# Kernel tuning notes

Hardware: AMD Instinct MI355X
Metric: run time of the kernel (lower is better)

The kernel has to match this reference:

```python
import jax, jax.numpy as jnp
import numpy as np

N_HEADS, N_LEVELS, N_POINTS = 8, 4, 4


def _bilinear(im, grid, H, W):
    # im: [N, D, H*W] flattened level feature, grid: [N, Q, P, 2] in [-1, 1]
    # F.grid_sample bilinear, padding_mode='zeros', align_corners=False
    N, Q, P, _ = grid.shape
    D = im.shape[1]
    gx = ((grid[..., 0] + 1.0) * W - 1.0) * 0.5
    gy = ((grid[..., 1] + 1.0) * H - 1.0) * 0.5
    x0f = jnp.floor(gx)
    y0f = jnp.floor(gy)
    x0 = x0f.astype(jnp.int32)
    y0 = y0f.astype(jnp.int32)
    wx1 = gx - x0f
    wy1 = gy - y0f
    acc = jnp.zeros((N, D, Q * P), im.dtype)
    corners = ((0, 0, (1 - wx1) * (1 - wy1)), (1, 0, wx1 * (1 - wy1)),
               (0, 1, (1 - wx1) * wy1), (1, 1, wx1 * wy1))
    for dx, dy, wgt in corners:
        xi = x0 + dx
        yi = y0 + dy
        valid = (xi >= 0) & (xi < W) & (yi >= 0) & (yi < H)
        idx = jnp.clip(yi, 0, H - 1) * W + jnp.clip(xi, 0, W - 1)
        v = jnp.take_along_axis(im, idx.reshape(N, 1, Q * P), axis=2)  # [N,D,QP]
        acc = acc + v * jnp.where(valid, wgt, 0.0).reshape(N, 1, Q * P)
    return acc.reshape(N, D, Q, P)


def _forward(query, value, reference_points, shapes_np,
             w_off, b_off, w_attn, b_attn, w_val, b_val, w_out, b_out):
    B, Q, E = query.shape
    H_, L, P = N_HEADS, N_LEVELS, N_POINTS
    D = E // H_
    v = (value @ w_val + b_val).reshape(B, -1, H_, D)  # [B, Nv, H, D]
    off = (query @ w_off + b_off).reshape(B, Q, H_, L, P, 2)
    attn = (query @ w_attn + b_attn).reshape(B, Q, H_, L * P)
    attn = jax.nn.softmax(attn, axis=-1).reshape(B, Q, H_, L, P)
    # offset_scale = [W_l, H_l] per level
    scale = jnp.asarray(np.stack([shapes_np[:, 1], shapes_np[:, 0]], -1), jnp.float32)
    locs = reference_points[:, :, None, :, None, :] + off / scale[None, None, None, :, None, :]
    grid = 2.0 * locs - 1.0  # [B, Q, H, L, P, 2]
    starts = np.concatenate([[0], np.cumsum(shapes_np[:, 0] * shapes_np[:, 1])]).astype(int)
    out = jnp.zeros((B * H_, D, Q), query.dtype)
    for lvl in range(L):
        h, w = int(shapes_np[lvl, 0]), int(shapes_np[lvl, 1])
        feat = v[:, starts[lvl]:starts[lvl + 1]]                      # [B, h*w, H, D]
        feat = feat.transpose(0, 2, 3, 1).reshape(B * H_, D, h * w)   # [BH, D, hw]
        g = jnp.transpose(grid[:, :, :, lvl], (0, 2, 1, 3, 4)).reshape(B * H_, Q, P, 2)
        sampled = _bilinear(feat, g, h, w)                            # [BH, D, Q, P]
        wl = jnp.transpose(attn[:, :, :, lvl], (0, 2, 1, 3)).reshape(B * H_, 1, Q, P)
        out = out + (sampled * wl).sum(-1)                            # [BH, D, Q]
    out = out.reshape(B, H_ * D, Q).transpose(0, 2, 1)                # [B, Q, E]
    return out @ w_out + b_out


def setup_inputs() -> dict:
    key = jax.random.key(0)
    ks = jax.random.split(key, 12)
    B, Q, E = 2, 19947, 256
    L, H_, P = N_LEVELS, N_HEADS, N_POINTS
    shapes = jnp.array([[100, 150], [50, 75], [25, 38], [13, 19]], dtype=jnp.int64)
    s = 0.02
    return {
        'query': jax.random.normal(ks[0], (B, Q, E), jnp.float32),
        'value': jax.random.normal(ks[1], (B, Q, E), jnp.float32),
        'reference_points': jax.random.uniform(ks[2], (B, Q, L, 2), jnp.float32),
        'spatial_shapes': shapes,
        'w_off': jax.random.normal(ks[3], (E, H_ * L * P * 2), jnp.float32) * s,
        'b_off': jax.random.normal(ks[4], (H_ * L * P * 2,), jnp.float32) * s,
        'w_attn': jax.random.normal(ks[5], (E, H_ * L * P), jnp.float32) * s,
        'b_attn': jax.random.normal(ks[6], (H_ * L * P,), jnp.float32) * s,
        'w_val': jax.random.normal(ks[7], (E, E), jnp.float32) * s,
        'b_val': jax.random.normal(ks[8], (E,), jnp.float32) * s,
        'w_out': jax.random.normal(ks[9], (E, E), jnp.float32) * s,
        'b_out': jax.random.normal(ks[10], (E,), jnp.float32) * s,
    }


def reference(query, value, reference_points, spatial_shapes,
              w_off, b_off, w_attn, b_attn, w_val, b_val, w_out, b_out):
    shapes_np = np.asarray(spatial_shapes)
    return _forward(query, value, reference_points, shapes_np,
                    w_off, b_off, w_attn, b_attn, w_val, b_val, w_out, b_out)
```

## Files before the change

kernel.cpp:

```cpp
#include <hip/hip_runtime.h>
#include <math.h>

#define B_    2
#define Q_    19947
#define E_    256
#define H_    8
#define D_    32
#define L_    4
#define P_    4

typedef _Float16 f16_t;
typedef f16_t f16x8 __attribute__((ext_vector_type(8)));
typedef f16_t f16x4 __attribute__((ext_vector_type(4)));
typedef float f32x4 __attribute__((ext_vector_type(4)));

__global__ __launch_bounds__(256)
void transpose_all(const float* __restrict__ w_val, const float* __restrict__ w_off,
                   const float* __restrict__ w_attn, const float* __restrict__ w_out,
                   f16_t* __restrict__ WtV, f16_t* __restrict__ WtQ,
                   f16_t* __restrict__ WtO)
{
    const float* in; f16_t* out; int N;
    switch (blockIdx.z) {
        case 0:  in = w_val;  out = WtV;             N = 256; break;
        case 1:  in = w_off;  out = WtQ;             N = 256; break;
        case 2:  in = w_attn; out = WtQ + 256 * 256; N = 128; break;
        default: in = w_out;  out = WtO;             N = 256; break;
    }
    const int nt = blockIdx.x * 32;
    if (nt >= N) return;
    const int kt = blockIdx.y * 32;

    __shared__ float tile[32][33];
    const int x  = threadIdx.x & 31;
    const int y0 = threadIdx.x >> 5;
    #pragma unroll
    for (int p = 0; p < 4; ++p)
        tile[y0 + p * 8][x] = in[(size_t)(kt + y0 + p * 8) * N + nt + x];
    __syncthreads();
    const int kf = kt >> 5;
    #pragma unroll
    for (int p = 0; p < 4; ++p) {
        const int n    = nt + y0 + p * 8;
        const int nf   = n >> 4, l16 = n & 15;
        const int quad = (x >> 3) & 3, e = x & 7;
        out[(size_t)(nf * 8 + kf) * 512 + (quad * 16 + l16) * 8 + e]
            = (f16_t)tile[x][y0 + p * 8];
    }
}

__global__ __launch_bounds__(256, 4)
void gemm_proj(const float* __restrict__ Aval, const float* __restrict__ Aqry,
               const f16_t* __restrict__ WtV, const f16_t* __restrict__ WtQ,
               const float* __restrict__ b_val, const float* __restrict__ b_off,
               const float* __restrict__ b_attn,
               f16_t* __restrict__ v_proj, float* __restrict__ off_b,
               float* __restrict__ attn_b, int M)
{
    __shared__ __align__(16) f16_t As[32][264];

    const int t  = threadIdx.x;
    const int m0 = blockIdx.x * 32;
    const bool isVal = (blockIdx.y == 0);
    const float* __restrict__ Af = isVal ? Aval : Aqry;
    const f16_t* __restrict__ Wt = isVal ? WtV : WtQ;
    const int JW = isVal ? 4 : 6;

    {
        const int r  = t >> 3;
        const int c0 = (t & 7) * 32;
        const int gm = m0 + r;
        #pragma unroll
        for (int u = 0; u < 2; ++u) {
            f16_t tmp[16];
            if (gm < M) {
                #pragma unroll
                for (int q = 0; q < 4; ++q) {
                    const float4 v4 = *(const float4*)(Af + (size_t)gm * 256 + c0 + u * 16 + q * 4);
                    tmp[q*4+0] = (f16_t)v4.x; tmp[q*4+1] = (f16_t)v4.y;
                    tmp[q*4+2] = (f16_t)v4.z; tmp[q*4+3] = (f16_t)v4.w;
                }
            } else {
                #pragma unroll
                for (int q = 0; q < 16; ++q) tmp[q] = (f16_t)0.f;
            }
            *(f16x8*)&As[r][c0 + u * 16]     = *(const f16x8*)&tmp[0];
            *(f16x8*)&As[r][c0 + u * 16 + 8] = *(const f16x8*)&tmp[8];
        }
    }
    __syncthreads();

    const int lane = t & 63;
    const int w    = t >> 6;
    const int quad = lane >> 4, l16 = lane & 15;

    f16x8 af[2][8];
    #pragma unroll
    for (int mi = 0; mi < 2; ++mi)
        #pragma unroll
        for (int kf = 0; kf < 8; ++kf)
            af[mi][kf] = *(const f16x8*)&As[mi * 16 + l16][kf * 32 + quad * 8];

    for (int j = 0; j < JW; ++j) {
        const int nf = (isVal ? w * 4 : w * 6) + j;
        const f16_t* __restrict__ bp = Wt + (size_t)nf * 4096 + lane * 8;

        f32x4 acc0 = {0.f, 0.f, 0.f, 0.f};
        f32x4 acc1 = {0.f, 0.f, 0.f, 0.f};
        #pragma unroll
        for (int kf = 0; kf < 8; ++kf) {
            const f16x8 bfr = *(const f16x8*)(bp + kf * 512);
            acc0 = __builtin_amdgcn_mfma_f32_16x16x32_f16(af[0][kf], bfr, acc0, 0, 0, 0);
            acc1 = __builtin_amdgcn_mfma_f32_16x16x32_f16(af[1][kf], bfr, acc1, 0, 0, 0);
        }

        const int n  = nf * 16 + l16;
        const float bv = isVal ? b_val[n] : (n < 256 ? b_off[n] : b_attn[n - 256]);
        #pragma unroll
        for (int r = 0; r < 4; ++r) {
            const int gm0 = m0 + quad * 4 + r;
            const int gm1 = gm0 + 16;
            if (isVal) {
                if (gm0 < M) v_proj[(size_t)gm0 * 256 + n] = (f16_t)(acc0[r] + bv);
                if (gm1 < M) v_proj[(size_t)gm1 * 256 + n] = (f16_t)(acc1[r] + bv);
            } else if (n < 256) {
                if (gm0 < M) off_b[(size_t)gm0 * 256 + n] = acc0[r] + bv;
                if (gm1 < M) off_b[(size_t)gm1 * 256 + n] = acc1[r] + bv;
            } else {
                if (gm0 < M) attn_b[(size_t)gm0 * 128 + (n - 256)] = acc0[r] + bv;
                if (gm1 < M) attn_b[(size_t)gm1 * 128 + (n - 256)] = acc1[r] + bv;
            }
        }
    }
}

__global__ __launch_bounds__(256, 4)
void msda_fused(const f16_t* __restrict__ v,
                const float* __restrict__ off,
                const float* __restrict__ attn,
                const float* __restrict__ ref,
                const f16_t* __restrict__ WoT,
                const float* __restrict__ b_out,
                float* __restrict__ out,
                int BQ)
{
    constexpr int SH[4] = {100, 50, 25, 13};
    constexpr int SW[4] = {150, 75, 38, 19};
    constexpr int ST[4] = {0, 15000, 18750, 19700};

    __shared__ __align__(16) f16_t Samp[16][264];

    const int t   = threadIdx.x;
    const int bq0 = blockIdx.x * 16;

    #pragma unroll
    for (int r = 0; r < 2; ++r) {
        const int g    = t >> 2;
        const int qi   = (g >> 3) + r * 8;
        const int h    = g & 7;
        const int lane = t & 3;
        const int bq   = bq0 + qi;

        float acc[8] = {0.f, 0.f, 0.f, 0.f, 0.f, 0.f, 0.f, 0.f};

        if (bq < BQ) {
            const int b = bq / Q_;
            const f16_t* vbase = v + ((size_t)b * Q_) * E_ + h * D_ + lane * 8;
            const float* offp  = off  + (size_t)bq * 256 + h * 32;
            const float* attnp = attn + (size_t)bq * 128 + h * 16;

            float aw[16];
            #pragma unroll
            for (int i = 0; i < 4; ++i) {
                const float4 x = *(const float4*)(attnp + i * 4);
                aw[i*4+0] = x.x; aw[i*4+1] = x.y; aw[i*4+2] = x.z; aw[i*4+3] = x.w;
            }
            float mx = aw[0];
            #pragma unroll
            for (int i = 1; i < 16; ++i) mx = fmaxf(mx, aw[i]);
            float sum = 0.f;
            #pragma unroll
            for (int i = 0; i < 16; ++i) { aw[i] = expf(aw[i] - mx); sum += aw[i]; }
            const float inv = 1.f / sum;
            #pragma unroll
            for (int i = 0; i < 16; ++i) aw[i] *= inv;

            const float4 r01 = *(const float4*)(ref + (size_t)bq * 8);
            const float4 r23 = *(const float4*)(ref + (size_t)bq * 8 + 4);
            const float rx[4] = {r01.x, r01.z, r23.x, r23.z};
            const float ry[4] = {r01.y, r01.w, r23.y, r23.w};

            #pragma unroll
            for (int l = 0; l < L_; ++l) {
                const float fW = (float)SW[l], fH = (float)SH[l];
                const int   Ww = SW[l], Hh = SH[l], st = ST[l];
                #pragma unroll
                for (int pp = 0; pp < 2; ++pp) {
                    const float4 o2 = *(const float4*)(offp + l * 8 + pp * 4);
                    #pragma unroll
                    for (int q = 0; q < 2; ++q) {
                        const int   p  = pp * 2 + q;
                        const float ox = q ? o2.z : o2.x;
                        const float oy = q ? o2.w : o2.y;
                        const float wA = aw[l * 4 + p];
                        const float gx = fmaf(rx[l], fW, ox) - 0.5f;
                        const float gy = fmaf(ry[l], fH, oy) - 0.5f;
                        const float x0f = floorf(gx), y0f = floorf(gy);
                        const int   x0  = (int)x0f,   y0  = (int)y0f;
                        const float wx1 = gx - x0f,   wy1 = gy - y0f;
                        const float wx0 = 1.f - wx1,  wy0 = 1.f - wy1;

                        const float mxw0 = ((unsigned)x0     < (unsigned)Ww) ? wx0 : 0.f;
                        const float mxw1 = ((unsigned)(x0+1) < (unsigned)Ww) ? wx1 : 0.f;
                        const float myw0 = ((unsigned)y0     < (unsigned)Hh) ? wy0 : 0.f;
                        const float myw1 = ((unsigned)(y0+1) < (unsigned)Hh) ? wy1 : 0.f;
                        const int xc0 = min(max(x0, 0),     Ww - 1);
                        const int xc1 = min(max(x0 + 1, 0), Ww - 1);
                        const int yc0 = min(max(y0, 0),     Hh - 1);
                        const int yc1 = min(max(y0 + 1, 0), Hh - 1);

                        const float w00 = wA * mxw0 * myw0;
                        const float w10 = wA * mxw1 * myw0;
                        const float w01 = wA * mxw0 * myw1;
                        const float w11 = wA * mxw1 * myw1;

                        const f16x8 s00 = *(const f16x8*)(vbase + (size_t)(st + yc0 * Ww + xc0) * E_);
                        const f16x8 s10 = *(const f16x8*)(vbase + (size_t)(st + yc0 * Ww + xc1) * E_);
                        const f16x8 s01 = *(const f16x8*)(vbase + (size_t)(st + yc1 * Ww + xc0) * E_);
                        const f16x8 s11 = *(const f16x8*)(vbase + (size_t)(st + yc1 * Ww + xc1) * E_);

                        #pragma unroll
                        for (int c = 0; c < 8; ++c) {
                            acc[c] = fmaf(w00, (float)s00[c], acc[c]);
                            acc[c] = fmaf(w10, (float)s10[c], acc[c]);
                            acc[c] = fmaf(w01, (float)s01[c], acc[c]);
                            acc[c] = fmaf(w11, (float)s11[c], acc[c]);
                        }
                    }
                }
            }
        }

        f16x8 o;
        #pragma unroll
        for (int c = 0; c < 8; ++c) o[c] = (f16_t)acc[c];
        *(f16x8*)&Samp[qi][h * 32 + lane * 8] = o;
    }

    __syncthreads();

    const int lane = t & 63;
    const int w    = t >> 6;
    const int quad = lane >> 4, l16 = lane & 15;

    f16x8 af[8];
    #pragma unroll
    for (int kf = 0; kf < 8; ++kf)
        af[kf] = *(const f16x8*)&Samp[l16][kf * 32 + quad * 8];

    f32x4 acc4[4];
    #pragma unroll
    for (int j = 0; j < 4; ++j) {
        f32x4 z = {0.f, 0.f, 0.f, 0.f};
        acc4[j] = z;
    }

    #pragma unroll
    for (int j = 0; j < 4; ++j) {
        const int nf = w * 4 + j;
        const f16_t* bp = WoT + (size_t)nf * 4096 + lane * 8;
        #pragma unroll
        for (int kf = 0; kf < 8; ++kf) {
            const f16x8 bfr = *(const f16x8*)(bp + kf * 512);
            acc4[j] = __builtin_amdgcn_mfma_f32_16x16x32_f16(af[kf], bfr, acc4[j], 0, 0, 0);
        }
    }

    #pragma unroll
    for (int j = 0; j < 4; ++j) {
        const int n  = w * 64 + j * 16 + l16;
        const float bv = b_out[n];
        #pragma unroll
        for (int r = 0; r < 4; ++r) {
            const int gm = bq0 + quad * 4 + r;
            if (gm < BQ)
                out[(size_t)gm * 256 + n] = acc4[j][r] + bv;
        }
    }
}

extern "C" void kernel_launch(void* const* d_in, const int* in_sizes, int n_in,
                              void* d_out, int out_size, void* d_ws, size_t ws_size,
                              hipStream_t stream)
{
    const float* query  = (const float*)d_in[0];
    const float* value  = (const float*)d_in[1];
    const float* refpts = (const float*)d_in[2];
    const float* w_off  = (const float*)d_in[4];
    const float* b_off  = (const float*)d_in[5];
    const float* w_attn = (const float*)d_in[6];
    const float* b_attn = (const float*)d_in[7];
    const float* w_val  = (const float*)d_in[8];
    const float* b_val  = (const float*)d_in[9];
    const float* w_out  = (const float*)d_in[10];
    const float* b_out  = (const float*)d_in[11];
    float* out = (float*)d_out;

    const int BQ = B_ * Q_;

    char* ws = (char*)d_ws;
    f16_t* v_proj = (f16_t*)ws;                       ws += (size_t)BQ * 256 * 2;
    float* off_b  = (float*)ws;                       ws += (size_t)BQ * 256 * 4;
    float* attn_b = (float*)ws;                       ws += (size_t)BQ * 128 * 4;
    f16_t* WtV    = (f16_t*)ws;                       ws += (size_t)256 * 256 * 2;
    f16_t* WtQ    = (f16_t*)ws;                       ws += (size_t)384 * 256 * 2;
    f16_t* WtO    = (f16_t*)ws;

    const dim3 blk(256);

    transpose_all<<<dim3(8, 8, 4), blk, 0, stream>>>(w_val, w_off, w_attn, w_out,
                                                     WtV, WtQ, WtO);

    const int mg32 = (BQ + 31) / 32;

    gemm_proj<<<dim3(mg32, 2), blk, 0, stream>>>(
        value, query, WtV, WtQ, b_val, b_off, b_attn,
        v_proj, off_b, attn_b, BQ);

    const int mg16 = (BQ + 15) / 16;
    msda_fused<<<dim3(mg16), blk, 0, stream>>>(
        v_proj, off_b, attn_b, refpts, WtO, b_out, out, BQ);
}
```

Measured before the change: 271.5 us.

## Assign one thread per (query, head) and double queries per block in MSDA

The sampling stage now gives each thread a whole (query, head) pair with 32 channels, instead of four threads each handling 8 channels. Each block covers 32 queries, and the output GEMM loops over two 16-row tiles. This removes the redundant per-lane softmax and bilinear coordinate math and halves the number of blocks. Index math is switched to 32-bit unsigned, and softmax uses exp2f. The cost is more registers per thread (32 accumulators), fewer threads in flight per sample, and less coalesced gathers, which may lower occupancy.

```diff
diff --git a/kernel.cpp b/kernel.cpp
--- a/kernel.cpp
+++ b/kernel.cpp
@@ -147,27 +147,29 @@
     constexpr int SH[4] = {100, 50, 25, 13};
     constexpr int SW[4] = {150, 75, 38, 19};
     constexpr int ST[4] = {0, 15000, 18750, 19700};
-
-    __shared__ __align__(16) f16_t Samp[16][264];
+    constexpr float LOG2E = 1.4426950408889634f;
+
+    __shared__ __align__(16) f16_t Samp[32][264];
 
     const int t   = threadIdx.x;
-    const int bq0 = blockIdx.x * 16;
-
-    #pragma unroll
-    for (int r = 0; r < 2; ++r) {
-        const int g    = t >> 2;
-        const int qi   = (g >> 3) + r * 8;
-        const int h    = g & 7;
-        const int lane = t & 3;
-        const int bq   = bq0 + qi;
-
-        float acc[8] = {0.f, 0.f, 0.f, 0.f, 0.f, 0.f, 0.f, 0.f};
+    const int bq0 = blockIdx.x * 32;
+
+    {
+        const int qi = t >> 3;
+        const int h  = t & 7;
+        const int bq = bq0 + qi;
+
+        float acc[32];
+        #pragma unroll
+        for (int c = 0; c < 32; ++c) acc[c] = 0.f;
 
         if (bq < BQ) {
-            const int b = bq / Q_;
-            const f16_t* vbase = v + ((size_t)b * Q_) * E_ + h * D_ + lane * 8;
-            const float* offp  = off  + (size_t)bq * 256 + h * 32;
-            const float* attnp = attn + (size_t)bq * 128 + h * 16;
+            const f16x8* __restrict__ vp = (const f16x8*)v;
+            const unsigned hoff = (unsigned)(h * 4)
+                                + (bq >= Q_ ? (unsigned)(Q_ * (E_ / 8)) : 0u);
+
+            const float* __restrict__ offp  = off  + (size_t)bq * 256 + h * 32;
+            const float* __restrict__ attnp = attn + (size_t)bq * 128 + h * 16;
 
             float aw[16];
             #pragma unroll
@@ -178,9 +180,13 @@
             float mx = aw[0];
             #pragma unroll
             for (int i = 1; i < 16; ++i) mx = fmaxf(mx, aw[i]);
+            const float mb = mx * LOG2E;
             float sum = 0.f;
             #pragma unroll
-            for (int i = 0; i < 16; ++i) { aw[i] = expf(aw[i] - mx); sum += aw[i]; }
+            for (int i = 0; i < 16; ++i) {
+                aw[i] = exp2f(fmaf(aw[i], LOG2E, -mb));
+                sum += aw[i];
+            }
             const float inv = 1.f / sum;
             #pragma unroll
             for (int i = 0; i < 16; ++i) aw[i] *= inv;
@@ -224,27 +230,39 @@
                         const float w01 = wA * mxw0 * myw1;
                         const float w11 = wA * mxw1 * myw1;
 
-                        const f16x8 s00 = *(const f16x8*)(vbase + (size_t)(st + yc0 * Ww + xc0) * E_);
-                        const f16x8 s10 = *(const f16x8*)(vbase + (size_t)(st + yc0 * Ww + xc1) * E_);
-                        const f16x8 s01 = *(const f16x8*)(vbase + (size_t)(st + yc1 * Ww + xc0) * E_);
-                        const f16x8 s11 = *(const f16x8*)(vbase + (size_t)(st + yc1 * Ww + xc1) * E_);
+                        const unsigned r0 = (unsigned)(st + yc0 * Ww);
+                        const unsigned r1 = (unsigned)(st + yc1 * Ww);
+                        const unsigned i00 = (r0 + (unsigned)xc0) * 32u + hoff;
+                        const unsigned i10 = (r0 + (unsigned)xc1) * 32u + hoff;
+                        const unsigned i01 = (r1 + (unsigned)xc0) * 32u + hoff;
+                        const unsigned i11 = (r1 + (unsigned)xc1) * 32u + hoff;
 
                         #pragma unroll
-                        for (int c = 0; c < 8; ++c) {
-                            acc[c] = fmaf(w00, (float)s00[c], acc[c]);
-                            acc[c] = fmaf(w10, (float)s10[c], acc[c]);
-                            acc[c] = fmaf(w01, (float)s01[c], acc[c]);
-                            acc[c] = fmaf(w11, (float)s11[c], acc[c]);
+                        for (int u = 0; u < 4; ++u) {
+                            const f16x8 s00 = vp[i00 + (unsigned)u];
+                            const f16x8 s10 = vp[i10 + (unsigned)u];
+                            const f16x8 s01 = vp[i01 + (unsigned)u];
+                            const f16x8 s11 = vp[i11 + (unsigned)u];
+                            #pragma unroll
+                            for (int c = 0; c < 8; ++c) {
+                                acc[u*8+c] = fmaf(w00, (float)s00[c], acc[u*8+c]);
+                                acc[u*8+c] = fmaf(w10, (float)s10[c], acc[u*8+c]);
+                                acc[u*8+c] = fmaf(w01, (float)s01[c], acc[u*8+c]);
+                                acc[u*8+c] = fmaf(w11, (float)s11[c], acc[u*8+c]);
+                            }
                         }
                     }
                 }
             }
         }
 
-        f16x8 o;
-        #pragma unroll
-        for (int c = 0; c < 8; ++c) o[c] = (f16_t)acc[c];
-        *(f16x8*)&Samp[qi][h * 32 + lane * 8] = o;
+        #pragma unroll
+        for (int u = 0; u < 4; ++u) {
+            f16x8 o;
+            #pragma unroll
+            for (int c = 0; c < 8; ++c) o[c] = (f16_t)acc[u*8+c];
+            *(f16x8*)&Samp[qi][h * 32 + u * 8] = o;
+        }
     }
 
     __syncthreads();
@@ -253,38 +271,31 @@
     const int w    = t >> 6;
     const int quad = lane >> 4, l16 = lane & 15;
 
-    f16x8 af[8];
     #pragma unroll
-    for (int kf = 0; kf < 8; ++kf)
-        af[kf] = *(const f16x8*)&Samp[l16][kf * 32 + quad * 8];
-
-    f32x4 acc4[4];
-    #pragma unroll
-    for (int j = 0; j < 4; ++j) {
-        f32x4 z = {0.f, 0.f, 0.f, 0.f};
-        acc4[j] = z;
-    }
-
-    #pragma unroll
-    for (int j = 0; j < 4; ++j) {
-        const int nf = w * 4 + j;
-        const f16_t* bp = WoT + (size_t)nf * 4096 + lane * 8;
-        #pragma unroll
-        for (int kf = 0; kf < 8; ++kf) {
-            const f16x8 bfr = *(const f16x8*)(bp + kf * 512);
-            acc4[j] = __builtin_amdgcn_mfma_f32_16x16x32_f16(af[kf], bfr, acc4[j], 0, 0, 0);
-        }
-    }
-
-    #pragma unroll
-    for (int j = 0; j < 4; ++j) {
-        const int n  = w * 64 + j * 16 + l16;
-        const float bv = b_out[n];
-        #pragma unroll
-        for (int r = 0; r < 4; ++r) {
-            const int gm = bq0 + quad * 4 + r;
-            if (gm < BQ)
-                out[(size_t)gm * 256 + n] = acc4[j][r] + bv;
+    for (int mi = 0; mi < 2; ++mi) {
+        f16x8 af[8];
+        #pragma unroll
+        for (int kf = 0; kf < 8; ++kf)
+            af[kf] = *(const f16x8*)&Samp[mi * 16 + l16][kf * 32 + quad * 8];
+
+        #pragma unroll
+        for (int j = 0; j < 4; ++j) {
+            const int nf = w * 4 + j;
+            const f16_t* bp = WoT + (size_t)nf * 4096 + lane * 8;
+            f32x4 a4 = {0.f, 0.f, 0.f, 0.f};
+            #pragma unroll
+            for (int kf = 0; kf < 8; ++kf) {
+                const f16x8 bfr = *(const f16x8*)(bp + kf * 512);
+                a4 = __builtin_amdgcn_mfma_f32_16x16x32_f16(af[kf], bfr, a4, 0, 0, 0);
+            }
+            const int n  = nf * 16 + l16;
+            const float bv = b_out[n];
+            #pragma unroll
+            for (int r = 0; r < 4; ++r) {
+                const int gm = bq0 + mi * 16 + quad * 4 + r;
+                if (gm < BQ)
+                    out[(size_t)gm * 256 + n] = a4[r] + bv;
+            }
         }
     }
 }
@@ -327,7 +338,6 @@
         value, query, WtV, WtQ, b_val, b_off, b_attn,
         v_proj, off_b, attn_b, BQ);
 
-    const int mg16 = (BQ + 15) / 16;
-    msda_fused<<<dim3(mg16), blk, 0, stream>>>(
+    msda_fused<<<dim3(mg32), blk, 0, stream>>>(
         v_proj, off_b, attn_b, refpts, WtO, b_out, out, BQ);
 }
```

Result: slower. 722.4 us (+166.1%).
